# Kernel tuning notes

Measured on AMD Instinct MI355X. Metric: run time of the kernel, lower is better.

The kernel has to match this reference:

```python
import jax, jax.numpy as jnp
import numpy as np

N_NODES = 150000
N_EDGES = 300000
N_GRAPHS = 6000
HID = 256


def _lin_init(key, fan_in, fan_out):
    k1, k2 = jax.random.split(key)
    s = 1.0 / np.sqrt(fan_in)
    W = jax.random.uniform(k1, (fan_in, fan_out), jnp.float32, -s, s)
    b = jax.random.uniform(k2, (fan_out,), jnp.float32, -s, s)
    return W, b


def setup_inputs() -> dict:
    key = jax.random.key(0)
    ks = jax.random.split(key, 16)
    x = jax.random.normal(ks[0], (N_NODES, 7), jnp.float32)
    edge_index = jax.random.randint(ks[1], (2, N_EDGES), 0, N_NODES, jnp.int64)
    batch = jnp.sort(jax.random.randint(ks[2], (N_NODES,), 0, N_GRAPHS, jnp.int64))
    inp = {"x": x, "edge_index": edge_index, "batch": batch}
    dims_in = [7, HID, HID, HID]
    for i in range(4):
        Wa, ba = _lin_init(ks[3 + 2 * i], dims_in[i], HID)
        Wb, bb = _lin_init(ks[4 + 2 * i], HID, HID)
        inp[f"W{i+1}a"], inp[f"b{i+1}a"] = Wa, ba
        inp[f"W{i+1}b"], inp[f"b{i+1}b"] = Wb, bb
    inp["Wh1"], inp["bh1"] = _lin_init(ks[11], HID, 128)
    inp["Wh2"], inp["bh2"] = _lin_init(ks[12], 128, 3)
    return inp


def _gin_layer(x, src, dst, Wa, ba, Wb, bb):
    # sum-aggregate neighbor features: messages from src scattered to dst
    agg = jax.ops.segment_sum(x[src], dst, num_segments=N_NODES)
    h = agg + x  # (1 + eps) * x with eps = 0
    h = jax.nn.relu(h @ Wa + ba) @ Wb + bb  # GIN MLP
    return jax.nn.relu(h)  # outer F.relu in forward


def reference(x, edge_index, batch,
              W1a, b1a, W1b, b1b,
              W2a, b2a, W2b, b2b,
              W3a, b3a, W3b, b3b,
              W4a, b4a, W4b, b4b,
              Wh1, bh1, Wh2, bh2):
    src, dst = edge_index[0], edge_index[1]
    h = _gin_layer(x, src, dst, W1a, b1a, W1b, b1b)
    h = _gin_layer(h, src, dst, W2a, b2a, W2b, b2b)
    h = _gin_layer(h, src, dst, W3a, b3a, W3b, b3b)
    h = _gin_layer(h, src, dst, W4a, b4a, W4b, b4b)
    # global mean pool per graph
    sums = jax.ops.segment_sum(h, batch, num_segments=N_GRAPHS)
    counts = jax.ops.segment_sum(jnp.ones((N_NODES,), h.dtype), batch, num_segments=N_GRAPHS)
    pooled = sums / jnp.maximum(counts, 1.0)[:, None]
    # head (Dropout is identity in eval mode)
    out = jax.nn.relu(pooled @ Wh1 + bh1) @ Wh2 + bh2
    return out
```

## Files before the change

kernel.cpp:

```cpp
#include <hip/hip_runtime.h>

using bf16x8 = __attribute__((ext_vector_type(8))) __bf16;
using bf16x4 = __attribute__((ext_vector_type(4))) __bf16;
using f32x4  = __attribute__((ext_vector_type(4))) float;

#define MN    150000
#define NEDGE 300000
#define NG    6000
#define NSCAN 586

__device__ __forceinline__ float loadF(const void* p, size_t i, int f32) {
    return f32 ? ((const float*)p)[i] : (float)((const __bf16*)p)[i];
}
__device__ __forceinline__ int loadI(const int* p, size_t i, int i64) {
    return i64 ? p[2 * i] : p[i];
}

__global__ void k_probe(const void* W1a, const int* ei, const int* batch, int* flags) {
    __shared__ int s_f32, s_einz, s_bnz;
    if (threadIdx.x == 0) { s_f32 = 0; s_einz = 0; s_bnz = 0; }
    __syncthreads();
    const unsigned short* w = (const unsigned short*)W1a;
    for (int i = threadIdx.x; i < 1792; i += 256) {
        int e = (w[i] >> 7) & 0xFF;
        if (e >= 0xF0) s_f32 = 1;
    }
    for (int i = threadIdx.x; i < 2048; i += 256)
        if (ei[2 * i + 1] != 0) s_einz = 1;
    for (int i = threadIdx.x; i < 2048; i += 256)
        if (batch[75000 + 2 * i + 1] != 0) s_bnz = 1;
    __syncthreads();
    if (threadIdx.x == 0) {
        flags[0] = s_f32;
        flags[1] = s_einz ? 0 : 1;
        flags[2] = s_bnz ? 0 : 1;
    }
}

__global__ void k_cvtWT(const void* W0, const void* W1, const void* W2, const void* W3,
                        const void* W4, const void* W5, const void* W6,
                        __bf16* __restrict__ Wt, const int* __restrict__ flags) {
    int j = blockIdx.x >> 8;
    int n = blockIdx.x & 255, k = threadIdx.x;
    const void* Ws[7] = {W0, W1, W2, W3, W4, W5, W6};
    Wt[(size_t)j * 65536 + (size_t)n * 256 + k] = (__bf16)loadF(Ws[j], (size_t)k * 256 + n, flags[0]);
}

__global__ void k_deg(const int* __restrict__ ei, int* __restrict__ cnt, int nE,
                      const int* __restrict__ flags) {
    int e = blockIdx.x * 256 + threadIdx.x;
    if (e >= nE) return;
    int i64 = flags[1];
    int d = loadI(ei, (size_t)nE + e, i64);
    if ((unsigned)d >= (unsigned)MN) d = 0;
    atomicAdd(&cnt[d], 1);
}
__global__ void k_blksum(const int* __restrict__ cnt, int* __restrict__ bsum, int n) {
    __shared__ int s[256];
    int t = threadIdx.x;
    int i = blockIdx.x * 256 + t;
    s[t] = (i < n) ? cnt[i] : 0;
    __syncthreads();
    for (int o = 128; o > 0; o >>= 1) {
        if (t < o) s[t] += s[t + o];
        __syncthreads();
    }
    if (t == 0) bsum[blockIdx.x] = s[0];
}
__global__ __launch_bounds__(1024) void k_scanb(const int* __restrict__ bsum,
                                                int* __restrict__ bbase, int nb) {
    __shared__ int s[1024];
    int t = threadIdx.x;
    int v = (t < nb) ? bsum[t] : 0;
    s[t] = v;
    __syncthreads();
#pragma unroll
    for (int o = 1; o < 1024; o <<= 1) {
        int x = (t >= o) ? s[t - o] : 0;
        __syncthreads();
        s[t] += x;
        __syncthreads();
    }
    if (t < nb) bbase[t] = s[t] - v;
}
__global__ void k_blkscan(const int* __restrict__ cnt, const int* __restrict__ bbase,
                          int* __restrict__ offs, int n) {
    __shared__ int s[256];
    int t = threadIdx.x;
    int i = blockIdx.x * 256 + t;
    int v = (i < n) ? cnt[i] : 0;
    s[t] = v;
    __syncthreads();
    for (int o = 1; o < 256; o <<= 1) {
        int x = (t >= o) ? s[t - o] : 0;
        __syncthreads();
        s[t] += x;
        __syncthreads();
    }
    if (i < n) offs[i] = bbase[blockIdx.x] + s[t] - v;
}
__global__ void k_fill(const int* __restrict__ ei, const int* __restrict__ offs,
                       int* __restrict__ cur, int* __restrict__ elist, int nE,
                       const int* __restrict__ flags) {
    int e = blockIdx.x * 256 + threadIdx.x;
    if (e >= nE) return;
    int i64 = flags[1];
    int s = loadI(ei, (size_t)e, i64);
    int d = loadI(ei, (size_t)nE + e, i64);
    if ((unsigned)s >= (unsigned)MN) s = 0;
    if ((unsigned)d >= (unsigned)MN) d = 0;
    int pos = offs[d] + atomicAdd(&cur[d], 1);
    if ((unsigned)pos < (unsigned)NEDGE) elist[pos] = s;
}

__global__ __launch_bounds__(256) void k_l1lite(
    const void* __restrict__ x, const int* __restrict__ offs,
    const int* __restrict__ deg, const int* __restrict__ elist,
    float* __restrict__ agg7, const int* __restrict__ flags, int M_) {
    int f32 = flags[0];
    int t = threadIdx.x;
    int v = blockIdx.x * 32 + (t >> 3);
    int j = t & 7;
    if (v >= M_ || j >= 7) return;
    float s = loadF(x, (size_t)v * 7 + j, f32);
    int b = offs[v], d = min(deg[v], 1024);
    for (int e = 0; e < d; ++e) {
        int u = elist[b + e];
        if ((unsigned)u >= (unsigned)MN) u = 0;
        s += loadF(x, (size_t)u * 7 + j, f32);
    }
    agg7[(size_t)v * 8 + j] = s;
}

template<int CI, int MI>
__device__ __forceinline__ void gemm_core(const __bf16* lA, const __bf16* __restrict__ WT,
                                          int n0, int lm, int lq, f32x4 acc[CI][MI]) {
    const __bf16* wp = WT + (size_t)(n0 + lm) * 256 + lq * 8;
    bf16x8 wf[CI], wn[CI];
#pragma unroll
    for (int ci = 0; ci < CI; ++ci)
        wf[ci] = *(const bf16x8*)(wp + ci * 16 * 256);
#pragma unroll
    for (int kt = 0; kt < 8; ++kt) {
        if (kt < 7) {
#pragma unroll
            for (int ci = 0; ci < CI; ++ci)
                wn[ci] = *(const bf16x8*)(wp + ci * 16 * 256 + (kt + 1) * 32);
        }
        int sw = (((kt * 4 + lq) ^ (lm & 7)) << 3);
        bf16x8 xf[MI];
#pragma unroll
        for (int mi = 0; mi < MI; ++mi)
            xf[mi] = *(const bf16x8*)(lA + (mi * 16 + lm) * 256 + sw);
#pragma unroll
        for (int ci = 0; ci < CI; ++ci)
#pragma unroll
            for (int mi = 0; mi < MI; ++mi)
                acc[ci][mi] = __builtin_amdgcn_mfma_f32_16x16x32_bf16(
                    wf[ci], xf[mi], acc[ci][mi], 0, 0, 0);
#pragma unroll
        for (int ci = 0; ci < CI; ++ci) wf[ci] = wn[ci];
    }
}

template<int CI, int MI>
__device__ __forceinline__ void epi_to_lds(__bf16* lA, f32x4 acc[CI][MI], const void* bias,
                                           int n0, int lm, int lq, int f32) {
#pragma unroll
    for (int ci = 0; ci < CI; ++ci) {
        int n4 = n0 + ci * 16 + lq * 4;
        float b0 = loadF(bias, n4 + 0, f32), b1 = loadF(bias, n4 + 1, f32);
        float b2 = loadF(bias, n4 + 2, f32), b3 = loadF(bias, n4 + 3, f32);
#pragma unroll
        for (int mi = 0; mi < MI; ++mi) {
            int m = mi * 16 + lm;
            f32x4 a = acc[ci][mi];
            bf16x4 v;
            v[0] = (__bf16)fmaxf(a[0] + b0, 0.f);
            v[1] = (__bf16)fmaxf(a[1] + b1, 0.f);
            v[2] = (__bf16)fmaxf(a[2] + b2, 0.f);
            v[3] = (__bf16)fmaxf(a[3] + b3, 0.f);
            *(bf16x4*)(lA + m * 256 + (((n4 >> 3) ^ (m & 7)) << 3) + (n4 & 7)) = v;
        }
    }
}

template<int RW>
__device__ __forceinline__ void lds_to_global(const __bf16* lA, __bf16* __restrict__ Y,
                                              int bm, int w, int lane, int M_) {
    int half = lane >> 5;
    int cc = lane & 31;
#pragma unroll
    for (int it = 0; it < RW / 2; ++it) {
        int r = w * RW + it * 2 + half;
        int gm = bm + r;
        if (gm < M_) {
            bf16x8 v = *(const bf16x8*)(lA + r * 256 + ((cc ^ (r & 7)) << 3));
            *(bf16x8*)(Y + (size_t)gm * 256 + cc * 8) = v;
        }
    }
}

__device__ __forceinline__ void stage128_agg512(const __bf16* __restrict__ H, __bf16* lA,
                                                const int* __restrict__ offs,
                                                const int* __restrict__ deg,
                                                const int* __restrict__ elist,
                                                int bm, int t, int M_) {
    int tc = t & 7;
    int rl = t >> 3;
#pragma unroll 1
    for (int p = 0; p < 2; ++p) {
        int r = p * 64 + rl;
        int gr = bm + r;
        if (gr >= M_) gr = M_ - 1;
        const __bf16* self = H + (size_t)gr * 256 + tc * 32;
        float acc[32];
        {
            bf16x8 v0 = *(const bf16x8*)(self + 0);
            bf16x8 v1 = *(const bf16x8*)(self + 8);
            bf16x8 v2 = *(const bf16x8*)(self + 16);
            bf16x8 v3 = *(const bf16x8*)(self + 24);
#pragma unroll
            for (int j = 0; j < 8; ++j) {
                acc[j]      = (float)v0[j];
                acc[8 + j]  = (float)v1[j];
                acc[16 + j] = (float)v2[j];
                acc[24 + j] = (float)v3[j];
            }
        }
        int b = offs[gr], d = min(deg[gr], 1024);
        int e = 0;
        for (; e + 1 < d; e += 2) {
            int u0 = elist[b + e];
            int u1 = elist[b + e + 1];
            if ((unsigned)u0 >= (unsigned)MN) u0 = 0;
            if ((unsigned)u1 >= (unsigned)MN) u1 = 0;
            const __bf16* nb0 = H + (size_t)u0 * 256 + tc * 32;
            const __bf16* nb1 = H + (size_t)u1 * 256 + tc * 32;
            bf16x8 a0 = *(const bf16x8*)(nb0 + 0);
            bf16x8 a1 = *(const bf16x8*)(nb0 + 8);
            bf16x8 a2 = *(const bf16x8*)(nb0 + 16);
            bf16x8 a3 = *(const bf16x8*)(nb0 + 24);
            bf16x8 c0 = *(const bf16x8*)(nb1 + 0);
            bf16x8 c1 = *(const bf16x8*)(nb1 + 8);
            bf16x8 c2 = *(const bf16x8*)(nb1 + 16);
            bf16x8 c3 = *(const bf16x8*)(nb1 + 24);
#pragma unroll
            for (int j = 0; j < 8; ++j) {
                acc[j]      += (float)a0[j] + (float)c0[j];
                acc[8 + j]  += (float)a1[j] + (float)c1[j];
                acc[16 + j] += (float)a2[j] + (float)c2[j];
                acc[24 + j] += (float)a3[j] + (float)c3[j];
            }
        }
        if (e < d) {
            int u = elist[b + e];
            if ((unsigned)u >= (unsigned)MN) u = 0;
            const __bf16* nb = H + (size_t)u * 256 + tc * 32;
            bf16x8 n0 = *(const bf16x8*)(nb + 0);
            bf16x8 n1 = *(const bf16x8*)(nb + 8);
            bf16x8 n2 = *(const bf16x8*)(nb + 16);
            bf16x8 n3 = *(const bf16x8*)(nb + 24);
#pragma unroll
            for (int j = 0; j < 8; ++j) {
                acc[j]      += (float)n0[j];
                acc[8 + j]  += (float)n1[j];
                acc[16 + j] += (float)n2[j];
                acc[24 + j] += (float)n3[j];
            }
        }
#pragma unroll
        for (int q = 0; q < 4; ++q) {
            int c = tc * 4 + q;
            bf16x8 o;
#pragma unroll
            for (int j = 0; j < 8; ++j) o[j] = (__bf16)acc[q * 8 + j];
            *(bf16x8*)(lA + r * 256 + ((c ^ (r & 7)) << 3)) = o;
        }
    }
}

__global__ __launch_bounds__(512, 4) void k_agg_mlp(
    const __bf16* __restrict__ H, const int* __restrict__ offs, const int* __restrict__ deg,
    const int* __restrict__ elist,
    const __bf16* __restrict__ WaT, const void* __restrict__ ba,
    const __bf16* __restrict__ WbT, const void* __restrict__ bb,
    __bf16* __restrict__ Y, const int* __restrict__ batch,
    float* __restrict__ pool, float* __restrict__ cntf, int do_pool,
    int M_, const int* __restrict__ flags) {
    __shared__ __align__(16) __bf16 lA[128 * 256];
    __shared__ int sbatch[128];
    int t = threadIdx.x;
    int f32 = flags[0];
    int bm = blockIdx.x * 128;
    int w = t >> 6, lane = t & 63, lm = lane & 15, lq = lane >> 4;
    int n0 = w * 32;

    stage128_agg512(H, lA, offs, deg, elist, bm, t, M_);
    if (do_pool && t < 128) {
        int gm = bm + t;
        sbatch[t] = (gm < M_) ? loadI(batch, gm, flags[2]) : -1;
    }
    __syncthreads();

    {
        f32x4 acc[2][8] = {};
        gemm_core<2, 8>(lA, WaT, n0, lm, lq, acc);
        __syncthreads();
        epi_to_lds<2, 8>(lA, acc, ba, n0, lm, lq, f32);
    }
    __syncthreads();

    f32x4 acc2[2][8] = {};
    gemm_core<2, 8>(lA, WbT, n0, lm, lq, acc2);
    __syncthreads();
    epi_to_lds<2, 8>(lA, acc2, bb, n0, lm, lq, f32);
    __syncthreads();

    if (!do_pool) {
        lds_to_global<16>(lA, Y, bm, w, lane, M_);
    } else {
        int c = t & 255;
        int h2 = t >> 8;
        int g = -1;
        float acc = 0.f, run = 0.f;
        int rbeg = h2 * 64;
        for (int r = rbeg; r < rbeg + 64; ++r) {
            int bg = sbatch[r];
            if (bg < 0) break;
            if ((unsigned)bg >= (unsigned)NG) bg = 0;
            float v = (float)lA[r * 256 + (((c >> 3) ^ (r & 7)) << 3) + (c & 7)];
            if (bg != g) {
                if (g >= 0) {
                    atomicAdd(&pool[(size_t)g * 256 + c], acc);
                    if (c == 0) atomicAdd(&cntf[g], run);
                }
                g = bg; acc = 0.f; run = 0.f;
            }
            acc += v; run += 1.f;
        }
        if (g >= 0) {
            atomicAdd(&pool[(size_t)g * 256 + c], acc);
            if (c == 0) atomicAdd(&cntf[g], run);
        }
    }
}

__global__ __launch_bounds__(512, 4) void k_gemm1(
    const float* __restrict__ agg7, const void* __restrict__ W1a, const void* __restrict__ b1a,
    const __bf16* __restrict__ WT, const void* __restrict__ bias,
    __bf16* __restrict__ Y, int M_, const int* __restrict__ flags) {
    __shared__ __align__(16) __bf16 lA[128 * 256];
    __shared__ float sW[7 * 256];
    __shared__ float sB[256];
    int t = threadIdx.x;
    int f32 = flags[0];
    int bm = blockIdx.x * 128;
    int w = t >> 6, lane = t & 63, lm = lane & 15, lq = lane >> 4;
    int n0 = w * 32;

    if (t < 256) sB[t] = loadF(b1a, t, f32);
    for (int i = t; i < 7 * 256; i += 512) sW[i] = loadF(W1a, i, f32);
    __syncthreads();

    {
        int r = t >> 2;
        int gr = bm + r;
        if (gr >= M_) gr = M_ - 1;
        float a[7];
#pragma unroll
        for (int k = 0; k < 7; ++k) a[k] = agg7[(size_t)gr * 8 + k];
        int c0 = (t & 3) * 64;
#pragma unroll
        for (int s8 = 0; s8 < 8; ++s8) {
            bf16x8 o;
#pragma unroll
            for (int j = 0; j < 8; ++j) {
                int cc = c0 + s8 * 8 + j;
                float v = sB[cc];
#pragma unroll
                for (int k = 0; k < 7; ++k) v = fmaf(a[k], sW[k * 256 + cc], v);
                o[j] = (__bf16)fmaxf(v, 0.f);
            }
            int ch = (c0 >> 3) + s8;
            *(bf16x8*)(lA + r * 256 + ((ch ^ (r & 7)) << 3)) = o;
        }
    }
    __syncthreads();

    f32x4 acc[2][8] = {};
    gemm_core<2, 8>(lA, WT, n0, lm, lq, acc);
    __syncthreads();
    epi_to_lds<2, 8>(lA, acc, bias, n0, lm, lq, f32);
    __syncthreads();
    lds_to_global<16>(lA, Y, bm, w, lane, M_);
}

__global__ __launch_bounds__(512) void k_head(
    const float* __restrict__ pool, const float* __restrict__ cnt,
    const void* __restrict__ Wh1, const void* __restrict__ bh1,
    const void* __restrict__ Wh2, const void* __restrict__ bh2,
    void* __restrict__ outv, const int* __restrict__ flags) {
    int g = blockIdx.x, t = threadIdx.x;
    int f32 = flags[0];
    __shared__ float p[256];
    __shared__ float hidp[4][128];
    __shared__ float hid[128];
    float inv = 1.0f / fmaxf(cnt[g], 1.0f);
    if (t < 256) p[t] = pool[(size_t)g * 256 + t] * inv;
    __syncthreads();
    {
        int n = t & 127, kh = t >> 7;
        int kb = kh * 64;
        float s = 0.f;
#pragma unroll 8
        for (int k = 0; k < 64; ++k)
            s = fmaf(p[kb + k], loadF(Wh1, (size_t)(kb + k) * 128 + n, f32), s);
        hidp[kh][n] = s;
    }
    __syncthreads();
    if (t < 128)
        hid[t] = fmaxf(hidp[0][t] + hidp[1][t] + hidp[2][t] + hidp[3][t]
                       + loadF(bh1, t, f32), 0.f);
    __syncthreads();
    if (t < 192) {
        int n3 = t >> 6, lane = t & 63;
        float o = hid[lane] * loadF(Wh2, (size_t)lane * 3 + n3, f32);
        o = fmaf(hid[lane + 64], loadF(Wh2, (size_t)(lane + 64) * 3 + n3, f32), o);
#pragma unroll
        for (int off = 32; off > 0; off >>= 1) o += __shfl_down(o, off, 64);
        if (lane == 0) {
            o += loadF(bh2, n3, f32);
            if (f32) ((float*)outv)[(size_t)g * 3 + n3] = o;
            else     ((__bf16*)outv)[(size_t)g * 3 + n3] = (__bf16)o;
        }
    }
}

extern "C" void kernel_launch(void* const* d_in, const int* in_sizes, int n_in,
                              void* d_out, int out_size, void* d_ws, size_t ws_size,
                              hipStream_t stream) {
    const void* x     = d_in[0];
    const int*  ei    = (const int*)d_in[1];
    const int*  batch = (const int*)d_in[2];
    const void *W[4][2], *b[4][2];
    for (int l = 0; l < 4; ++l) {
        W[l][0] = d_in[3 + 4 * l];
        b[l][0] = d_in[4 + 4 * l];
        W[l][1] = d_in[5 + 4 * l];
        b[l][1] = d_in[6 + 4 * l];
    }
    const void* Wh1 = d_in[19];
    const void* bh1 = d_in[20];
    const void* Wh2 = d_in[21];
    const void* bh2 = d_in[22];

    char* p = (char*)d_ws;
    auto alloc = [&](size_t bytes) -> char* {
        char* r = p;
        p += (bytes + 255) & ~(size_t)255;
        return r;
    };
    __bf16* B1    = (__bf16*)alloc((size_t)MN * 256 * 2);
    __bf16* B2    = (__bf16*)alloc((size_t)MN * 256 * 2);
    __bf16* WT    = (__bf16*)alloc((size_t)7 * 256 * 256 * 2);
    float*  AGG7  = (float*)alloc((size_t)MN * 8 * 4);
    int*    offs  = (int*)alloc((size_t)MN * 4);
    int*    cnt   = (int*)alloc((size_t)MN * 4);
    int*    elist = (int*)alloc((size_t)NEDGE * 4);
    int*    bsum  = (int*)alloc((size_t)NSCAN * 4);
    int*    bbase = (int*)alloc((size_t)NSCAN * 4);
    float*  POOL  = (float*)alloc((size_t)NG * 256 * 4);
    float*  CNTF  = (float*)alloc((size_t)NG * 4);
    int*    flags = (int*)alloc(64);

    k_probe<<<1, 256, 0, stream>>>(W[0][0], ei, batch, flags);

    k_cvtWT<<<7 * 256, 256, 0, stream>>>(W[0][1], W[1][0], W[1][1], W[2][0], W[2][1],
                                         W[3][0], W[3][1], WT, flags);

    hipMemsetAsync(cnt, 0, (size_t)MN * 4, stream);
    k_deg<<<(NEDGE + 255) / 256, 256, 0, stream>>>(ei, cnt, NEDGE, flags);
    k_blksum<<<NSCAN, 256, 0, stream>>>(cnt, bsum, MN);
    k_scanb<<<1, 1024, 0, stream>>>(bsum, bbase, NSCAN);
    k_blkscan<<<NSCAN, 256, 0, stream>>>(cnt, bbase, offs, MN);
    hipMemsetAsync(cnt, 0, (size_t)MN * 4, stream);
    k_fill<<<(NEDGE + 255) / 256, 256, 0, stream>>>(ei, offs, cnt, elist, NEDGE, flags);

    hipMemsetAsync(POOL, 0, (size_t)NG * 256 * 4 + (size_t)NG * 4, stream);

    int gblocks = (MN + 127) / 128;

    k_l1lite<<<(MN + 31) / 32, 256, 0, stream>>>(x, offs, cnt, elist, AGG7, flags, MN);
    k_gemm1<<<gblocks, 512, 0, stream>>>(AGG7, W[0][0], b[0][0], WT , b[0][1],
                                         B1, MN, flags);

    __bf16* bin = B1;
    __bf16* bout = B2;
    for (int l = 1; l < 4; ++l) {
        const __bf16* WaT = WT + (size_t)(1 + 2 * (l - 1)) * 65536;
        const __bf16* WbT = WT + (size_t)(2 + 2 * (l - 1)) * 65536;
        int dp = (l == 3) ? 1 : 0;
        k_agg_mlp<<<gblocks, 512, 0, stream>>>(bin, offs, cnt, elist,
                                               WaT, b[l][0], WbT, b[l][1], bout,
                                               batch, POOL, CNTF, dp, MN, flags);
        __bf16* tmp = bin; bin = bout; bout = tmp;
    }

    k_head<<<NG, 512, 0, stream>>>(POOL, CNTF, Wh1, bh1, Wh2, bh2, d_out, flags);
}
```

Measured before the change: 545.8 us.

## Replace three-pass scan with atomic wave allocation and fuse layer-1 aggregation into GEMM

The three-kernel prefix scan for CSR offsets is replaced by one kernel that does a wave-level shuffle scan and claims each wave's base offset with an atomic on a global counter. Neighbour lists stay contiguous per node, but their order in elist is no longer sorted by node id. The separate layer-1 7-feature aggregation kernel is removed, and each gemm1 thread now gathers its own neighbours' input features directly. This cuts kernel launches and the AGG7 intermediate, at the cost of four threads per row redundantly gathering the same neighbours inside gemm1.

```diff
diff --git a/kernel.cpp b/kernel.cpp
--- a/kernel.cpp
+++ b/kernel.cpp
@@ -46,59 +46,35 @@
     Wt[(size_t)j * 65536 + (size_t)n * 256 + k] = (__bf16)loadF(Ws[j], (size_t)k * 256 + n, flags[0]);
 }
 
-__global__ void k_deg(const int* __restrict__ ei, int* __restrict__ cnt, int nE,
-                      const int* __restrict__ flags) {
+__global__ void k_deg(const int* __restrict__ ei, int* __restrict__ cnt, int* __restrict__ total,
+                      int nE, const int* __restrict__ flags) {
     int e = blockIdx.x * 256 + threadIdx.x;
+    if (blockIdx.x == 0 && threadIdx.x == 0) *total = 0;
     if (e >= nE) return;
     int i64 = flags[1];
     int d = loadI(ei, (size_t)nE + e, i64);
     if ((unsigned)d >= (unsigned)MN) d = 0;
     atomicAdd(&cnt[d], 1);
 }
-__global__ void k_blksum(const int* __restrict__ cnt, int* __restrict__ bsum, int n) {
-    __shared__ int s[256];
-    int t = threadIdx.x;
-    int i = blockIdx.x * 256 + t;
-    s[t] = (i < n) ? cnt[i] : 0;
-    __syncthreads();
-    for (int o = 128; o > 0; o >>= 1) {
-        if (t < o) s[t] += s[t + o];
-        __syncthreads();
-    }
-    if (t == 0) bsum[blockIdx.x] = s[0];
-}
-__global__ __launch_bounds__(1024) void k_scanb(const int* __restrict__ bsum,
-                                                int* __restrict__ bbase, int nb) {
-    __shared__ int s[1024];
-    int t = threadIdx.x;
-    int v = (t < nb) ? bsum[t] : 0;
-    s[t] = v;
-    __syncthreads();
-#pragma unroll
-    for (int o = 1; o < 1024; o <<= 1) {
-        int x = (t >= o) ? s[t - o] : 0;
-        __syncthreads();
-        s[t] += x;
-        __syncthreads();
-    }
-    if (t < nb) bbase[t] = s[t] - v;
-}
-__global__ void k_blkscan(const int* __restrict__ cnt, const int* __restrict__ bbase,
-                          int* __restrict__ offs, int n) {
-    __shared__ int s[256];
-    int t = threadIdx.x;
-    int i = blockIdx.x * 256 + t;
-    int v = (i < n) ? cnt[i] : 0;
-    s[t] = v;
-    __syncthreads();
-    for (int o = 1; o < 256; o <<= 1) {
-        int x = (t >= o) ? s[t - o] : 0;
-        __syncthreads();
-        s[t] += x;
-        __syncthreads();
-    }
-    if (i < n) offs[i] = bbase[blockIdx.x] + s[t] - v;
-}
+
+__global__ void k_alloc(const int* __restrict__ cnt, int* __restrict__ offs,
+                        int* __restrict__ total, int n) {
+    int v = blockIdx.x * 256 + threadIdx.x;
+    int lane = threadIdx.x & 63;
+    int d = (v < n) ? cnt[v] : 0;
+    int x = d;
+#pragma unroll
+    for (int o = 1; o < 64; o <<= 1) {
+        int y = __shfl_up(x, o, 64);
+        if (lane >= o) x += y;
+    }
+    int wsum = __shfl(x, 63, 64);
+    int base = 0;
+    if (lane == 63) base = atomicAdd(total, wsum);
+    base = __shfl(base, 63, 64);
+    if (v < n) offs[v] = base + x - d;
+}
+
 __global__ void k_fill(const int* __restrict__ ei, const int* __restrict__ offs,
                        int* __restrict__ cur, int* __restrict__ elist, int nE,
                        const int* __restrict__ flags) {
@@ -111,25 +87,6 @@
     if ((unsigned)d >= (unsigned)MN) d = 0;
     int pos = offs[d] + atomicAdd(&cur[d], 1);
     if ((unsigned)pos < (unsigned)NEDGE) elist[pos] = s;
-}
-
-__global__ __launch_bounds__(256) void k_l1lite(
-    const void* __restrict__ x, const int* __restrict__ offs,
-    const int* __restrict__ deg, const int* __restrict__ elist,
-    float* __restrict__ agg7, const int* __restrict__ flags, int M_) {
-    int f32 = flags[0];
-    int t = threadIdx.x;
-    int v = blockIdx.x * 32 + (t >> 3);
-    int j = t & 7;
-    if (v >= M_ || j >= 7) return;
-    float s = loadF(x, (size_t)v * 7 + j, f32);
-    int b = offs[v], d = min(deg[v], 1024);
-    for (int e = 0; e < d; ++e) {
-        int u = elist[b + e];
-        if ((unsigned)u >= (unsigned)MN) u = 0;
-        s += loadF(x, (size_t)u * 7 + j, f32);
-    }
-    agg7[(size_t)v * 8 + j] = s;
 }
 
 template<int CI, int MI>
@@ -347,7 +304,9 @@
 }
 
 __global__ __launch_bounds__(512, 4) void k_gemm1(
-    const float* __restrict__ agg7, const void* __restrict__ W1a, const void* __restrict__ b1a,
+    const void* __restrict__ x, const int* __restrict__ offs, const int* __restrict__ deg,
+    const int* __restrict__ elist,
+    const void* __restrict__ W1a, const void* __restrict__ b1a,
     const __bf16* __restrict__ WT, const void* __restrict__ bias,
     __bf16* __restrict__ Y, int M_, const int* __restrict__ flags) {
     __shared__ __align__(16) __bf16 lA[128 * 256];
@@ -369,7 +328,14 @@
         if (gr >= M_) gr = M_ - 1;
         float a[7];
 #pragma unroll
-        for (int k = 0; k < 7; ++k) a[k] = agg7[(size_t)gr * 8 + k];
+        for (int k = 0; k < 7; ++k) a[k] = loadF(x, (size_t)gr * 7 + k, f32);
+        int b = offs[gr], d = min(deg[gr], 1024);
+        for (int e = 0; e < d; ++e) {
+            int u = elist[b + e];
+            if ((unsigned)u >= (unsigned)MN) u = 0;
+#pragma unroll
+            for (int k = 0; k < 7; ++k) a[k] += loadF(x, (size_t)u * 7 + k, f32);
+        }
         int c0 = (t & 3) * 64;
 #pragma unroll
         for (int s8 = 0; s8 < 8; ++s8) {
@@ -464,12 +430,10 @@
     __bf16* B1    = (__bf16*)alloc((size_t)MN * 256 * 2);
     __bf16* B2    = (__bf16*)alloc((size_t)MN * 256 * 2);
     __bf16* WT    = (__bf16*)alloc((size_t)7 * 256 * 256 * 2);
-    float*  AGG7  = (float*)alloc((size_t)MN * 8 * 4);
     int*    offs  = (int*)alloc((size_t)MN * 4);
     int*    cnt   = (int*)alloc((size_t)MN * 4);
     int*    elist = (int*)alloc((size_t)NEDGE * 4);
-    int*    bsum  = (int*)alloc((size_t)NSCAN * 4);
-    int*    bbase = (int*)alloc((size_t)NSCAN * 4);
+    int*    TOTAL = (int*)alloc(64);
     float*  POOL  = (float*)alloc((size_t)NG * 256 * 4);
     float*  CNTF  = (float*)alloc((size_t)NG * 4);
     int*    flags = (int*)alloc(64);
@@ -480,10 +444,8 @@
                                          W[3][0], W[3][1], WT, flags);
 
     hipMemsetAsync(cnt, 0, (size_t)MN * 4, stream);
-    k_deg<<<(NEDGE + 255) / 256, 256, 0, stream>>>(ei, cnt, NEDGE, flags);
-    k_blksum<<<NSCAN, 256, 0, stream>>>(cnt, bsum, MN);
-    k_scanb<<<1, 1024, 0, stream>>>(bsum, bbase, NSCAN);
-    k_blkscan<<<NSCAN, 256, 0, stream>>>(cnt, bbase, offs, MN);
+    k_deg<<<(NEDGE + 255) / 256, 256, 0, stream>>>(ei, cnt, TOTAL, NEDGE, flags);
+    k_alloc<<<NSCAN, 256, 0, stream>>>(cnt, offs, TOTAL, MN);
     hipMemsetAsync(cnt, 0, (size_t)MN * 4, stream);
     k_fill<<<(NEDGE + 255) / 256, 256, 0, stream>>>(ei, offs, cnt, elist, NEDGE, flags);
 
@@ -491,8 +453,8 @@
 
     int gblocks = (MN + 127) / 128;
 
-    k_l1lite<<<(MN + 31) / 32, 256, 0, stream>>>(x, offs, cnt, elist, AGG7, flags, MN);
-    k_gemm1<<<gblocks, 512, 0, stream>>>(AGG7, W[0][0], b[0][0], WT , b[0][1],
+    k_gemm1<<<gblocks, 512, 0, stream>>>(x, offs, cnt, elist,
+                                         W[0][0], b[0][0], WT , b[0][1],
                                          B1, MN, flags);
 
     __bf16* bin = B1;
```

New measurement: 563.3 us. 1.03x slower.
